# Kernel tuning notes

Measured on AMD Instinct MI355X. Metric: run time of the kernel, lower is better.

## Reference

```python
import jax, jax.numpy as jnp
import numpy as np

B, T, C = 8, 2048, 1024
NEG_BIG = -1e30  # exp(NEG_BIG - row_max) underflows to exactly 0 in fp32


def setup_inputs() -> dict:
    key = jax.random.key(0)
    k1, k2 = jax.random.split(key)
    x = jax.random.normal(k1, (B, T, C), dtype=jnp.float32)
    # nn.Linear weight, shape [out, in]; forward computes x @ W^T
    W_H = jax.random.normal(k2, (C, C), dtype=jnp.float32) * (1.0 / np.sqrt(C))
    return {"x": x, "W_H": W_H}


def reference(x, W_H):
    Tdim = x.shape[1]
    xH = jnp.einsum('btc,dc->btd', x, W_H)          # H(x) = x @ W^T, [B,T,C]
    scores = jnp.einsum('btc,bsc->bts', x, xH)       # bilinear scores, [B,T,T]
    # tril_plus_one=True -> strictly-lower-triangular mask (diagonal=-1)
    mask = jnp.tril(jnp.ones((Tdim, Tdim), dtype=bool), k=-1)
    scores = jnp.where(mask, scores, NEG_BIG)
    wei = jax.nn.softmax(scores, axis=-1)            # fully-masked rows -> uniform, zeroed below
    all_masked = ~mask.any(axis=-1)                  # [T], True for row 0
    wei = jnp.where(all_masked[None, :, None], 0.0, wei)
    out = jnp.einsum('bts,bsc->btc', wei, xH)
    return -out
```

## Files before the change

### kernel.cpp

```cpp
#include <hip/hip_runtime.h>
#include <stdint.h>

#define Bn 8
#define Tn 2048
#define Cn 1024
#define Mn (Bn * Tn)
#define NTRI 136

typedef __attribute__((ext_vector_type(4))) float f32x4;
typedef _Float16 f16;
typedef __attribute__((ext_vector_type(8))) _Float16 f16x8;
typedef uint16_t u16;
typedef uint32_t u32;

static __device__ __forceinline__ u16 f2h(float f) {
  union { f16 h; u16 u; } c; c.h = (f16)f; return c.u;
}
static __device__ __forceinline__ f32x4 mfmaH(f16x8 a, f16x8 b, f32x4 c) {
  return __builtin_amdgcn_mfma_f32_16x16x32_f16(a, b, c, 0, 0, 0);
}
static __device__ __forceinline__ void gld16(const void* g, void* l) {
  __builtin_amdgcn_global_load_lds(
      (const __attribute__((address_space(1))) u32*)g,
      (__attribute__((address_space(3))) u32*)l, 16, 0, 0);
}

__global__ __launch_bounds__(256) void ksplitW(const float* __restrict__ s,
                                               u16* __restrict__ hi) {
  size_t i = ((size_t)blockIdx.x * 256 + threadIdx.x) * 8;
  float4 a = *(const float4*)(s + i), b = *(const float4*)(s + i + 4);
  float f[8] = {a.x, a.y, a.z, a.w, b.x, b.y, b.z, b.w};
  union { u16 u[8]; uint4 v; } H;
#pragma unroll
  for (int j = 0; j < 8; ++j) H.u[j] = f2h(f[j]);
  *(uint4*)(hi + i) = H.v;
}

__global__ __launch_bounds__(256) void ksplitX(const float* __restrict__ s,
                                               u16* __restrict__ hi,
                                               u16* __restrict__ lo) {
  size_t i = ((size_t)blockIdx.x * 256 + threadIdx.x) * 8;
  float4 a = *(const float4*)(s + i), b = *(const float4*)(s + i + 4);
  float f[8] = {a.x, a.y, a.z, a.w, b.x, b.y, b.z, b.w};
  union { u16 u[8]; uint4 v; } H, L;
#pragma unroll
  for (int j = 0; j < 8; ++j) {
    f16 h = (f16)f[j];
    union { f16 h; u16 u; } ch; ch.h = h;
    H.u[j] = ch.u;
    L.u[j] = f2h(f[j] - (float)h);
  }
  *(uint4*)(hi + i) = H.v;
  *(uint4*)(lo + i) = L.v;
}

__global__ __launch_bounds__(256) void k1_xh(const u16* __restrict__ x_h,
                                             const u16* __restrict__ W_h,
                                             u16* __restrict__ xh) {
  __shared__ __align__(16) u16 Ah[8192], Bh[8192];
  const int tid = threadIdx.x;
  const int m0 = blockIdx.x * 128, n0 = blockIdx.y * 128;
  const int wave = tid >> 6, lane = tid & 63;
  const int wrow = (wave >> 1) * 64, wcol = (wave & 1) * 64;
  const int quad = lane >> 4, l16 = lane & 15;

  f32x4 acc[4][4] = {};

  for (int k0 = 0; k0 < Cn; k0 += 64) {
#pragma unroll
    for (int i = 0; i < 4; ++i) {
      int chunk = i * 256 + tid;
      int kk = chunk >> 9, row = (chunk >> 2) & 127, c8 = (chunk & 3) * 8;
      gld16(x_h + (size_t)(m0 + row) * Cn + k0 + kk * 32 + c8, Ah + chunk * 8);
      gld16(W_h + (size_t)(n0 + row) * Cn + k0 + kk * 32 + c8, Bh + chunk * 8);
    }
    __syncthreads();
#pragma unroll
    for (int kk = 0; kk < 2; ++kk) {
      f16x8 a[4], b[4];
#pragma unroll
      for (int i = 0; i < 4; ++i) {
        a[i] = *(const f16x8*)(Ah + kk * 4096 + (wrow + i * 16 + l16) * 32 + quad * 8);
        b[i] = *(const f16x8*)(Bh + kk * 4096 + (wcol + i * 16 + l16) * 32 + quad * 8);
      }
#pragma unroll
      for (int mi = 0; mi < 4; ++mi)
#pragma unroll
        for (int ni = 0; ni < 4; ++ni)
          acc[mi][ni] = mfmaH(a[mi], b[ni], acc[mi][ni]);
    }
    __syncthreads();
  }
#pragma unroll
  for (int mi = 0; mi < 4; ++mi)
#pragma unroll
    for (int ni = 0; ni < 4; ++ni)
#pragma unroll
      for (int r = 0; r < 4; ++r) {
        int row = wrow + mi * 16 + quad * 4 + r;
        int col = wcol + ni * 16 + l16;
        xh[(size_t)(m0 + row) * Cn + n0 + col] = f2h(acc[mi][ni][r]);
      }
}

__global__ __launch_bounds__(256) void k2_scores(const u16* __restrict__ x_h,
                                                 const u16* __restrict__ x_l,
                                                 const u16* __restrict__ xh,
                                                 u16* __restrict__ P,
                                                 float* __restrict__ mt,
                                                 float* __restrict__ lt) {
  __shared__ __align__(16) union {
    struct { u16 Ah[4096], Al[4096], Bh[4096]; } s;
    struct { float Mrow[2][128]; float Lrow[2][128]; } e;
  } u;
  const int tid = threadIdx.x;
  const int bL = blockIdx.y;
  const int lin = blockIdx.x;
  int qt = 0;
  while ((qt + 1) * (qt + 2) / 2 <= lin) qt++;
  const int st = lin - qt * (qt + 1) / 2;
  const int t0 = qt * 128, s0 = st * 128;
  const int wave = tid >> 6, lane = tid & 63;
  const int wrow = (wave >> 1) * 64, wcol = (wave & 1) * 64;
  const int quad = lane >> 4, l16 = lane & 15;
  const int srow = tid >> 2, skc = (tid & 3) * 8;

  f32x4 acc[4][4] = {};
  const size_t aoff = ((size_t)bL * Tn + t0 + srow) * Cn + skc;
  const size_t boff = ((size_t)bL * Tn + s0 + srow) * Cn + skc;

  for (int k0 = 0; k0 < Cn; k0 += 32) {
#pragma unroll
    for (int i = 0; i < 2; ++i) {
      size_t ro = (size_t)i * 64 * Cn;
      int lo_ = i * 2048 + tid * 8;
      gld16(x_h + aoff + ro + k0, u.s.Ah + lo_);
      gld16(x_l + aoff + ro + k0, u.s.Al + lo_);
      gld16(xh + boff + ro + k0, u.s.Bh + lo_);
    }
    __syncthreads();
    f16x8 a_h[4], a_l[4], b_h[4];
#pragma unroll
    for (int i = 0; i < 4; ++i) {
      a_h[i] = *(const f16x8*)(u.s.Ah + (wrow + i * 16 + l16) * 32 + quad * 8);
      a_l[i] = *(const f16x8*)(u.s.Al + (wrow + i * 16 + l16) * 32 + quad * 8);
      b_h[i] = *(const f16x8*)(u.s.Bh + (wcol + i * 16 + l16) * 32 + quad * 8);
    }
#pragma unroll
    for (int mi = 0; mi < 4; ++mi)
#pragma unroll
      for (int ni = 0; ni < 4; ++ni) {
        acc[mi][ni] = mfmaH(a_h[mi], b_h[ni], acc[mi][ni]);
        acc[mi][ni] = mfmaH(a_l[mi], b_h[ni], acc[mi][ni]);
      }
    __syncthreads();
  }

  float rm[4][4];
#pragma unroll
  for (int mi = 0; mi < 4; ++mi)
#pragma unroll
    for (int r = 0; r < 4; ++r) {
      int row = wrow + mi * 16 + quad * 4 + r;
      float m = -1e30f;
#pragma unroll
      for (int ni = 0; ni < 4; ++ni) {
        int col = wcol + ni * 16 + l16;
        if (s0 + col >= t0 + row) acc[mi][ni][r] = -1e30f;
        m = fmaxf(m, acc[mi][ni][r]);
      }
      m = fmaxf(m, __shfl_xor(m, 1));
      m = fmaxf(m, __shfl_xor(m, 2));
      m = fmaxf(m, __shfl_xor(m, 4));
      m = fmaxf(m, __shfl_xor(m, 8));
      rm[mi][r] = m;
    }
  if (l16 == 0) {
#pragma unroll
    for (int mi = 0; mi < 4; ++mi)
#pragma unroll
      for (int r = 0; r < 4; ++r)
        u.e.Mrow[wave & 1][wrow + mi * 16 + quad * 4 + r] = rm[mi][r];
  }
  __syncthreads();
  float rs[4][4];
#pragma unroll
  for (int mi = 0; mi < 4; ++mi)
#pragma unroll
    for (int r = 0; r < 4; ++r) {
      int row = wrow + mi * 16 + quad * 4 + r;
      float m2 = fmaxf(u.e.Mrow[0][row], u.e.Mrow[1][row]);
      float s = 0.f;
#pragma unroll
      for (int ni = 0; ni < 4; ++ni) {
        int col = wcol + ni * 16 + l16;
        float p = (s0 + col < t0 + row) ? __expf(acc[mi][ni][r] - m2) : 0.0f;
        acc[mi][ni][r] = p;
        s += p;
      }
      s += __shfl_xor(s, 1);
      s += __shfl_xor(s, 2);
      s += __shfl_xor(s, 4);
      s += __shfl_xor(s, 8);
      rs[mi][r] = s;
      rm[mi][r] = m2;
    }
  if (l16 == 0) {
#pragma unroll
    for (int mi = 0; mi < 4; ++mi)
#pragma unroll
      for (int r = 0; r < 4; ++r)
        u.e.Lrow[wave & 1][wrow + mi * 16 + quad * 4 + r] = rs[mi][r];
  }
  __syncthreads();
  if ((wave & 1) == 0 && l16 == 0) {
#pragma unroll
    for (int mi = 0; mi < 4; ++mi)
#pragma unroll
      for (int r = 0; r < 4; ++r) {
        int row = wrow + mi * 16 + quad * 4 + r;
        size_t rI = (size_t)bL * Tn + t0 + row;
        mt[rI * 16 + st] = rm[mi][r];
        lt[rI * 16 + st] = u.e.Lrow[0][row] + u.e.Lrow[1][row];
      }
  }
  const size_t pbase = (size_t)(bL * NTRI + lin) * 16384;
#pragma unroll
  for (int mi = 0; mi < 4; ++mi)
#pragma unroll
    for (int ni = 0; ni < 4; ++ni)
#pragma unroll
      for (int r = 0; r < 4; ++r) {
        int row = wrow + mi * 16 + quad * 4 + r;
        int col = wcol + ni * 16 + l16;
        P[pbase + row * 128 + col] = f2h(acc[mi][ni][r]);
      }
}

__global__ __launch_bounds__(256) void k3_stats(const float* __restrict__ mt,
                                                const float* __restrict__ lt,
                                                float* __restrict__ Mr,
                                                float* __restrict__ Li) {
  int r = blockIdx.x * 256 + threadIdx.x;
  int t = r & (Tn - 1);
  int nt = (t == 0) ? 0 : (((t - 1) >> 7) + 1);
  float M = -1e30f;
  for (int i = 0; i < nt; ++i) M = fmaxf(M, mt[(size_t)r * 16 + i]);
  float L = 0.f;
  for (int i = 0; i < nt; ++i) L += lt[(size_t)r * 16 + i] * __expf(mt[(size_t)r * 16 + i] - M);
  Mr[r] = M;
  Li[r] = (L > 0.f) ? 1.f / L : 0.f;
}

__global__ __launch_bounds__(256) void ktr(const u16* __restrict__ src,
                                           u16* __restrict__ dst) {
  __shared__ __align__(16) u16 S[128 * 136];
  const int t0 = blockIdx.x * 128, c0 = blockIdx.y * 128, b = blockIdx.z;
  const int tid = threadIdx.x;
#pragma unroll
  for (int i = 0; i < 8; ++i) {
    int chunk = tid + i * 256;
    int row = chunk >> 4, c8 = (chunk & 15) * 8;
    uint4 v = *(const uint4*)(src + ((size_t)b * Tn + t0 + row) * Cn + c0 + c8);
    *(uint4*)(S + row * 136 + c8) = v;
  }
  __syncthreads();
#pragma unroll
  for (int i = 0; i < 8; ++i) {
    int chunk = tid + i * 256;
    int crow = chunk >> 4, t8 = (chunk & 15) * 8;
    union { u16 s[8]; uint4 v; } o;
#pragma unroll
    for (int j = 0; j < 8; ++j) o.s[j] = S[(t8 + j) * 136 + crow];
    *(uint4*)(dst + ((size_t)b * Cn + c0 + crow) * Tn + t0 + t8) = o.v;
  }
}

__global__ __launch_bounds__(256) void k4_out(const u16* __restrict__ P,
                                              const u16* __restrict__ xhT,
                                              const float* __restrict__ mt,
                                              const float* __restrict__ Mr,
                                              const float* __restrict__ Li,
                                              float* __restrict__ out) {
  __shared__ __align__(16) u16 Ap[8192], Bp[8192];
  const int tid = threadIdx.x;
  const int tt = 15 - blockIdx.x;
  const int cn = blockIdx.y, bL = blockIdx.z;
  const int t0 = tt * 128, c0 = cn * 128;
  const int wave = tid >> 6, lane = tid & 63;
  const int wrow = (wave >> 1) * 64, wcol = (wave & 1) * 64;
  const int quad = lane >> 4, l16 = lane & 15;

  f32x4 acc[4][4] = {};
  size_t rI[4]; float MrL[4], LiL[4];
#pragma unroll
  for (int mi = 0; mi < 4; ++mi) {
    rI[mi] = (size_t)bL * Tn + t0 + wrow + mi * 16 + l16;
    MrL[mi] = Mr[rI[mi]];
    LiL[mi] = Li[rI[mi]];
  }
  const size_t bbase = ((size_t)bL * Cn + c0) * Tn;

  for (int st = 0; st <= tt; ++st) {
    f16 ah[4];
#pragma unroll
    for (int mi = 0; mi < 4; ++mi)
      ah[mi] = (f16)(__expf(mt[rI[mi] * 16 + st] - MrL[mi]) * LiL[mi]);
    const size_t pbase = (size_t)(bL * NTRI + tt * (tt + 1) / 2 + st) * 16384;
#pragma unroll 1
    for (int kl = 0; kl < 128; kl += 64) {
#pragma unroll
      for (int i = 0; i < 4; ++i) {
        int chunk = i * 256 + tid;
        int kk = chunk >> 9, row = (chunk >> 2) & 127, c8 = (chunk & 3) * 8;
        gld16(P + pbase + (size_t)row * 128 + kl + kk * 32 + c8, Ap + chunk * 8);
        gld16(xhT + bbase + (size_t)row * Tn + st * 128 + kl + kk * 32 + c8, Bp + chunk * 8);
      }
      __syncthreads();
#pragma unroll
      for (int kk = 0; kk < 2; ++kk) {
        f16x8 a[4], b[4];
#pragma unroll
        for (int i = 0; i < 4; ++i) {
          a[i] = *(const f16x8*)(Ap + kk * 4096 + (wrow + i * 16 + l16) * 32 + quad * 8);
          f16x8 sv;
#pragma unroll
          for (int j = 0; j < 8; ++j) sv[j] = ah[i];
          a[i] = a[i] * sv;
          b[i] = *(const f16x8*)(Bp + kk * 4096 + (wcol + i * 16 + l16) * 32 + quad * 8);
        }
#pragma unroll
        for (int mi = 0; mi < 4; ++mi)
#pragma unroll
          for (int ni = 0; ni < 4; ++ni)
            acc[mi][ni] = mfmaH(a[mi], b[ni], acc[mi][ni]);
      }
      __syncthreads();
    }
  }
#pragma unroll
  for (int mi = 0; mi < 4; ++mi)
#pragma unroll
    for (int ni = 0; ni < 4; ++ni)
#pragma unroll
      for (int r = 0; r < 4; ++r) {
        int row = wrow + mi * 16 + quad * 4 + r;
        int col = wcol + ni * 16 + l16;
        out[((size_t)bL * Tn + t0 + row) * Cn + c0 + col] = -acc[mi][ni][r];
      }
}

extern "C" void kernel_launch(void* const* d_in, const int* in_sizes, int n_in,
                              void* d_out, int out_size, void* d_ws, size_t ws_size,
                              hipStream_t stream) {
  (void)in_sizes; (void)n_in; (void)out_size;
  const float* x = (const float*)d_in[0];
  const float* W = (const float*)d_in[1];
  float* out = (float*)d_out;

  const size_t FULL_NEED = 3ull * Mn * Cn * 2 + (size_t)Bn * NTRI * 16384 * 2 +
                           (size_t)Cn * Cn * 2 + 2ull * Mn * 16 * 4 + 2ull * Mn * 4;
  const int nch = (ws_size >= FULL_NEED) ? 1 : 2;
  const int nb = Bn / nch;
  const size_t rowsC = (size_t)nb * Tn;
  const size_t sA = rowsC * Cn * 2;

  char* p = (char*)d_ws;
  u16* x_h = (u16*)p; p += sA;
  u16* xLT = (u16*)p; p += sA;
  u16* xh  = (u16*)p; p += sA;
  u16* Pp  = (u16*)p; p += (size_t)nb * NTRI * 16384 * 2;
  u16* W_h = (u16*)p; p += (size_t)Cn * Cn * 2;
  float* mt = (float*)p; p += rowsC * 16 * 4;
  float* lt = (float*)p; p += rowsC * 16 * 4;
  float* Mr = (float*)p; p += rowsC * 4;
  float* Li = (float*)p; p += rowsC * 4;

  dim3 blk(256);
  ksplitW<<<dim3(Cn * Cn / 2048), blk, 0, stream>>>(W, W_h);
  for (int c = 0; c < nch; ++c) {
    const float* xc = x + (size_t)c * rowsC * Cn;
    float* oc = out + (size_t)c * rowsC * Cn;
    ksplitX<<<dim3((u32)(rowsC * Cn / 2048)), blk, 0, stream>>>(xc, x_h, xLT);
    k1_xh<<<dim3((u32)(rowsC / 128), Cn / 128), blk, 0, stream>>>(x_h, W_h, xh);
    k2_scores<<<dim3(NTRI, nb), blk, 0, stream>>>(x_h, xLT, xh, Pp, mt, lt);
    k3_stats<<<dim3((u32)(rowsC / 256)), blk, 0, stream>>>(mt, lt, Mr, Li);
    ktr<<<dim3(Tn / 128, Cn / 128, nb), blk, 0, stream>>>(xh, xLT);
    k4_out<<<dim3(16, Cn / 128, nb), blk, 0, stream>>>(Pp, xLT, mt, Mr, Li, oc);
  }
}
```

Baseline: 427.1 us.

## Widen GEMM tiles to 128x256 and repack score tiles as 128x256 blocks

Widens the N dimension of the xH projection, score and output GEMMs from 128 to 256, so each wave computes a 64x128 tile and reuses each A fragment across twice as many MFMAs. The triangular score tiling becomes 128x256 blocks (72 per batch instead of 136), which changes the P buffer layout, the per-row stats stride and the softmax reduction. The output kernel loops over 256-wide key blocks with a clipped trip count. The workspace-size fallback to two batch chunks is removed, and the larger accumulators raise register and LDS use, which may lower occupancy and waste work on masked half-blocks.

```diff
diff --git a/kernel.cpp b/kernel.cpp
--- a/kernel.cpp
+++ b/kernel.cpp
@@ -5,7 +5,8 @@
 #define Tn 2048
 #define Cn 1024
 #define Mn (Bn * Tn)
-#define NTRI 136
+#define NTB 72
+#define NST 8
 
 typedef __attribute__((ext_vector_type(4))) float f32x4;
 typedef _Float16 f16;
@@ -23,6 +24,10 @@
   __builtin_amdgcn_global_load_lds(
       (const __attribute__((address_space(1))) u32*)g,
       (__attribute__((address_space(3))) u32*)l, 16, 0, 0);
+}
+static __device__ __forceinline__ int tri_off(int qt) {
+  int a = qt >> 1;
+  return (qt & 1) ? (a + 1) * (a + 1) : a * (a + 1);
 }
 
 __global__ __launch_bounds__(256) void ksplitW(const float* __restrict__ s,
@@ -57,36 +62,42 @@
 __global__ __launch_bounds__(256) void k1_xh(const u16* __restrict__ x_h,
                                              const u16* __restrict__ W_h,
                                              u16* __restrict__ xh) {
-  __shared__ __align__(16) u16 Ah[8192], Bh[8192];
+  __shared__ __align__(16) u16 Ah[8192], Bh[16384];
   const int tid = threadIdx.x;
-  const int m0 = blockIdx.x * 128, n0 = blockIdx.y * 128;
+  const int m0 = blockIdx.x * 128, n0 = blockIdx.y * 256;
   const int wave = tid >> 6, lane = tid & 63;
-  const int wrow = (wave >> 1) * 64, wcol = (wave & 1) * 64;
+  const int wrow = (wave >> 1) * 64, wcol = (wave & 1) * 128;
   const int quad = lane >> 4, l16 = lane & 15;
 
-  f32x4 acc[4][4] = {};
+  f32x4 acc[4][8] = {};
 
   for (int k0 = 0; k0 < Cn; k0 += 64) {
 #pragma unroll
     for (int i = 0; i < 4; ++i) {
       int chunk = i * 256 + tid;
       int kk = chunk >> 9, row = (chunk >> 2) & 127, c8 = (chunk & 3) * 8;
-      gld16(x_h + (size_t)(m0 + row) * Cn + k0 + kk * 32 + c8, Ah + chunk * 8);
-      gld16(W_h + (size_t)(n0 + row) * Cn + k0 + kk * 32 + c8, Bh + chunk * 8);
+      gld16(x_h + (size_t)(m0 + row) * Cn + k0 + kk * 32 + c8, Ah + kk * 4096 + row * 32 + c8);
+    }
+#pragma unroll
+    for (int i = 0; i < 8; ++i) {
+      int chunk = i * 256 + tid;
+      int kk = chunk >> 10, row = (chunk >> 2) & 255, c8 = (chunk & 3) * 8;
+      gld16(W_h + (size_t)(n0 + row) * Cn + k0 + kk * 32 + c8, Bh + kk * 8192 + row * 32 + c8);
     }
     __syncthreads();
 #pragma unroll
     for (int kk = 0; kk < 2; ++kk) {
-      f16x8 a[4], b[4];
-#pragma unroll
-      for (int i = 0; i < 4; ++i) {
+      f16x8 a[4], b[8];
+#pragma unroll
+      for (int i = 0; i < 4; ++i)
         a[i] = *(const f16x8*)(Ah + kk * 4096 + (wrow + i * 16 + l16) * 32 + quad * 8);
-        b[i] = *(const f16x8*)(Bh + kk * 4096 + (wcol + i * 16 + l16) * 32 + quad * 8);
-      }
+#pragma unroll
+      for (int j = 0; j < 8; ++j)
+        b[j] = *(const f16x8*)(Bh + kk * 8192 + (wcol + j * 16 + l16) * 32 + quad * 8);
 #pragma unroll
       for (int mi = 0; mi < 4; ++mi)
 #pragma unroll
-        for (int ni = 0; ni < 4; ++ni)
+        for (int ni = 0; ni < 8; ++ni)
           acc[mi][ni] = mfmaH(a[mi], b[ni], acc[mi][ni]);
     }
     __syncthreads();
@@ -94,7 +105,7 @@
 #pragma unroll
   for (int mi = 0; mi < 4; ++mi)
 #pragma unroll
-    for (int ni = 0; ni < 4; ++ni)
+    for (int ni = 0; ni < 8; ++ni)
 #pragma unroll
       for (int r = 0; r < 4; ++r) {
         int row = wrow + mi * 16 + quad * 4 + r;
@@ -110,48 +121,53 @@
                                                  float* __restrict__ mt,
                                                  float* __restrict__ lt) {
   __shared__ __align__(16) union {
-    struct { u16 Ah[4096], Al[4096], Bh[4096]; } s;
+    struct { u16 Ah[4096], Al[4096], Bh[8192]; } s;
     struct { float Mrow[2][128]; float Lrow[2][128]; } e;
   } u;
   const int tid = threadIdx.x;
   const int bL = blockIdx.y;
   const int lin = blockIdx.x;
-  int qt = 0;
-  while ((qt + 1) * (qt + 2) / 2 <= lin) qt++;
-  const int st = lin - qt * (qt + 1) / 2;
-  const int t0 = qt * 128, s0 = st * 128;
+  int qt = 0, base = 0;
+  while (base + (qt >> 1) + 1 <= lin) { base += (qt >> 1) + 1; qt++; }
+  const int st2 = lin - base;
+  const int t0 = qt * 128, s0 = st2 * 256;
   const int wave = tid >> 6, lane = tid & 63;
-  const int wrow = (wave >> 1) * 64, wcol = (wave & 1) * 64;
+  const int wrow = (wave >> 1) * 64, wcol = (wave & 1) * 128;
   const int quad = lane >> 4, l16 = lane & 15;
-  const int srow = tid >> 2, skc = (tid & 3) * 8;
-
-  f32x4 acc[4][4] = {};
-  const size_t aoff = ((size_t)bL * Tn + t0 + srow) * Cn + skc;
-  const size_t boff = ((size_t)bL * Tn + s0 + srow) * Cn + skc;
+
+  f32x4 acc[4][8] = {};
 
   for (int k0 = 0; k0 < Cn; k0 += 32) {
 #pragma unroll
     for (int i = 0; i < 2; ++i) {
-      size_t ro = (size_t)i * 64 * Cn;
-      int lo_ = i * 2048 + tid * 8;
-      gld16(x_h + aoff + ro + k0, u.s.Ah + lo_);
-      gld16(x_l + aoff + ro + k0, u.s.Al + lo_);
-      gld16(xh + boff + ro + k0, u.s.Bh + lo_);
+      int chunk = i * 256 + tid;
+      int row = chunk >> 2, c8 = (chunk & 3) * 8;
+      size_t g = ((size_t)bL * Tn + t0 + row) * Cn + k0 + c8;
+      gld16(x_h + g, u.s.Ah + row * 32 + c8);
+      gld16(x_l + g, u.s.Al + row * 32 + c8);
+    }
+#pragma unroll
+    for (int i = 0; i < 4; ++i) {
+      int chunk = i * 256 + tid;
+      int row = chunk >> 2, c8 = (chunk & 3) * 8;
+      gld16(xh + ((size_t)bL * Tn + s0 + row) * Cn + k0 + c8, u.s.Bh + row * 32 + c8);
     }
     __syncthreads();
-    f16x8 a_h[4], a_l[4], b_h[4];
+    f16x8 a_h[4], a_l[4], b[8];
 #pragma unroll
     for (int i = 0; i < 4; ++i) {
       a_h[i] = *(const f16x8*)(u.s.Ah + (wrow + i * 16 + l16) * 32 + quad * 8);
       a_l[i] = *(const f16x8*)(u.s.Al + (wrow + i * 16 + l16) * 32 + quad * 8);
-      b_h[i] = *(const f16x8*)(u.s.Bh + (wcol + i * 16 + l16) * 32 + quad * 8);
-    }
+    }
+#pragma unroll
+    for (int j = 0; j < 8; ++j)
+      b[j] = *(const f16x8*)(u.s.Bh + (wcol + j * 16 + l16) * 32 + quad * 8);
 #pragma unroll
     for (int mi = 0; mi < 4; ++mi)
 #pragma unroll
-      for (int ni = 0; ni < 4; ++ni) {
-        acc[mi][ni] = mfmaH(a_h[mi], b_h[ni], acc[mi][ni]);
-        acc[mi][ni] = mfmaH(a_l[mi], b_h[ni], acc[mi][ni]);
+      for (int ni = 0; ni < 8; ++ni) {
+        acc[mi][ni] = mfmaH(a_h[mi], b[ni], acc[mi][ni]);
+        acc[mi][ni] = mfmaH(a_l[mi], b[ni], acc[mi][ni]);
       }
     __syncthreads();
   }
@@ -164,7 +180,7 @@
       int row = wrow + mi * 16 + quad * 4 + r;
       float m = -1e30f;
 #pragma unroll
-      for (int ni = 0; ni < 4; ++ni) {
+      for (int ni = 0; ni < 8; ++ni) {
         int col = wcol + ni * 16 + l16;
         if (s0 + col >= t0 + row) acc[mi][ni][r] = -1e30f;
         m = fmaxf(m, acc[mi][ni][r]);
@@ -192,7 +208,7 @@
       float m2 = fmaxf(u.e.Mrow[0][row], u.e.Mrow[1][row]);
       float s = 0.f;
 #pragma unroll
-      for (int ni = 0; ni < 4; ++ni) {
+      for (int ni = 0; ni < 8; ++ni) {
         int col = wcol + ni * 16 + l16;
         float p = (s0 + col < t0 + row) ? __expf(acc[mi][ni][r] - m2) : 0.0f;
         acc[mi][ni][r] = p;
@@ -220,20 +236,20 @@
       for (int r = 0; r < 4; ++r) {
         int row = wrow + mi * 16 + quad * 4 + r;
         size_t rI = (size_t)bL * Tn + t0 + row;
-        mt[rI * 16 + st] = rm[mi][r];
-        lt[rI * 16 + st] = u.e.Lrow[0][row] + u.e.Lrow[1][row];
-      }
-  }
-  const size_t pbase = (size_t)(bL * NTRI + lin) * 16384;
+        mt[rI * NST + st2] = rm[mi][r];
+        lt[rI * NST + st2] = u.e.Lrow[0][row] + u.e.Lrow[1][row];
+      }
+  }
+  const size_t pbase = (size_t)(bL * NTB + lin) * 32768;
 #pragma unroll
   for (int mi = 0; mi < 4; ++mi)
 #pragma unroll
-    for (int ni = 0; ni < 4; ++ni)
+    for (int ni = 0; ni < 8; ++ni)
 #pragma unroll
       for (int r = 0; r < 4; ++r) {
         int row = wrow + mi * 16 + quad * 4 + r;
         int col = wcol + ni * 16 + l16;
-        P[pbase + row * 128 + col] = f2h(acc[mi][ni][r]);
+        P[pbase + row * 256 + col] = f2h(acc[mi][ni][r]);
       }
 }
 
@@ -243,11 +259,11 @@
                                                 float* __restrict__ Li) {
   int r = blockIdx.x * 256 + threadIdx.x;
   int t = r & (Tn - 1);
-  int nt = (t == 0) ? 0 : (((t - 1) >> 7) + 1);
+  int nt = (t == 0) ? 0 : (((t - 1) >> 8) + 1);
   float M = -1e30f;
-  for (int i = 0; i < nt; ++i) M = fmaxf(M, mt[(size_t)r * 16 + i]);
+  for (int i = 0; i < nt; ++i) M = fmaxf(M, mt[(size_t)r * NST + i]);
   float L = 0.f;
-  for (int i = 0; i < nt; ++i) L += lt[(size_t)r * 16 + i] * __expf(mt[(size_t)r * 16 + i] - M);
+  for (int i = 0; i < nt; ++i) L += lt[(size_t)r * NST + i] * __expf(mt[(size_t)r * NST + i] - M);
   Mr[r] = M;
   Li[r] = (L > 0.f) ? 1.f / L : 0.f;
 }
@@ -282,16 +298,16 @@
                                               const float* __restrict__ Mr,
                                               const float* __restrict__ Li,
                                               float* __restrict__ out) {
-  __shared__ __align__(16) u16 Ap[8192], Bp[8192];
+  __shared__ __align__(16) u16 Ap[8192], Bp[16384];
   const int tid = threadIdx.x;
   const int tt = 15 - blockIdx.x;
   const int cn = blockIdx.y, bL = blockIdx.z;
-  const int t0 = tt * 128, c0 = cn * 128;
+  const int t0 = tt * 128, c0 = cn * 256;
   const int wave = tid >> 6, lane = tid & 63;
-  const int wrow = (wave >> 1) * 64, wcol = (wave & 1) * 64;
+  const int wrow = (wave >> 1) * 64, wcol = (wave & 1) * 128;
   const int quad = lane >> 4, l16 = lane & 15;
 
-  f32x4 acc[4][4] = {};
+  f32x4 acc[4][8] = {};
   size_t rI[4]; float MrL[4], LiL[4];
 #pragma unroll
   for (int mi = 0; mi < 4; ++mi) {
@@ -300,26 +316,35 @@
     LiL[mi] = Li[rI[mi]];
   }
   const size_t bbase = ((size_t)bL * Cn + c0) * Tn;
-
-  for (int st = 0; st <= tt; ++st) {
+  const int off = tri_off(tt);
+  const int kend = (tt + 1) * 128;
+
+  for (int st2 = 0; st2 <= (tt >> 1); ++st2) {
     f16 ah[4];
 #pragma unroll
     for (int mi = 0; mi < 4; ++mi)
-      ah[mi] = (f16)(__expf(mt[rI[mi] * 16 + st] - MrL[mi]) * LiL[mi]);
-    const size_t pbase = (size_t)(bL * NTRI + tt * (tt + 1) / 2 + st) * 16384;
+      ah[mi] = (f16)(__expf(mt[rI[mi] * NST + st2] - MrL[mi]) * LiL[mi]);
+    const size_t pbase = (size_t)(bL * NTB + off + st2) * 32768;
+    const int klim = min(256, kend - st2 * 256);
 #pragma unroll 1
-    for (int kl = 0; kl < 128; kl += 64) {
+    for (int kl = 0; kl < klim; kl += 64) {
 #pragma unroll
       for (int i = 0; i < 4; ++i) {
         int chunk = i * 256 + tid;
         int kk = chunk >> 9, row = (chunk >> 2) & 127, c8 = (chunk & 3) * 8;
-        gld16(P + pbase + (size_t)row * 128 + kl + kk * 32 + c8, Ap + chunk * 8);
-        gld16(xhT + bbase + (size_t)row * Tn + st * 128 + kl + kk * 32 + c8, Bp + chunk * 8);
+        gld16(P + pbase + (size_t)row * 256 + kl + kk * 32 + c8, Ap + kk * 4096 + row * 32 + c8);
+      }
+#pragma unroll
+      for (int i = 0; i < 8; ++i) {
+        int chunk = i * 256 + tid;
+        int kk = chunk >> 10, row = (chunk >> 2) & 255, c8 = (chunk & 3) * 8;
+        gld16(xhT + bbase + (size_t)row * Tn + st2 * 256 + kl + kk * 32 + c8,
+              Bp + kk * 8192 + row * 32 + c8);
       }
       __syncthreads();
 #pragma unroll
       for (int kk = 0; kk < 2; ++kk) {
-        f16x8 a[4], b[4];
+        f16x8 a[4], b[8];
 #pragma unroll
         for (int i = 0; i < 4; ++i) {
           a[i] = *(const f16x8*)(Ap + kk * 4096 + (wrow + i * 16 + l16) * 32 + quad * 8);
@@ -327,12 +352,14 @@
 #pragma unroll
           for (int j = 0; j < 8; ++j) sv[j] = ah[i];
           a[i] = a[i] * sv;
-          b[i] = *(const f16x8*)(Bp + kk * 4096 + (wcol + i * 16 + l16) * 32 + quad * 8);
         }
 #pragma unroll
+        for (int j = 0; j < 8; ++j)
+          b[j] = *(const f16x8*)(Bp + kk * 8192 + (wcol + j * 16 + l16) * 32 + quad * 8);
+#pragma unroll
         for (int mi = 0; mi < 4; ++mi)
 #pragma unroll
-          for (int ni = 0; ni < 4; ++ni)
+          for (int ni = 0; ni < 8; ++ni)
             acc[mi][ni] = mfmaH(a[mi], b[ni], acc[mi][ni]);
       }
       __syncthreads();
@@ -341,7 +368,7 @@
 #pragma unroll
   for (int mi = 0; mi < 4; ++mi)
 #pragma unroll
-    for (int ni = 0; ni < 4; ++ni)
+    for (int ni = 0; ni < 8; ++ni)
 #pragma unroll
       for (int r = 0; r < 4; ++r) {
         int row = wrow + mi * 16 + quad * 4 + r;
@@ -353,39 +380,28 @@
 extern "C" void kernel_launch(void* const* d_in, const int* in_sizes, int n_in,
                               void* d_out, int out_size, void* d_ws, size_t ws_size,
                               hipStream_t stream) {
-  (void)in_sizes; (void)n_in; (void)out_size;
+  (void)in_sizes; (void)n_in; (void)out_size; (void)ws_size;
   const float* x = (const float*)d_in[0];
   const float* W = (const float*)d_in[1];
   float* out = (float*)d_out;
 
-  const size_t FULL_NEED = 3ull * Mn * Cn * 2 + (size_t)Bn * NTRI * 16384 * 2 +
-                           (size_t)Cn * Cn * 2 + 2ull * Mn * 16 * 4 + 2ull * Mn * 4;
-  const int nch = (ws_size >= FULL_NEED) ? 1 : 2;
-  const int nb = Bn / nch;
-  const size_t rowsC = (size_t)nb * Tn;
-  const size_t sA = rowsC * Cn * 2;
-
   char* p = (char*)d_ws;
-  u16* x_h = (u16*)p; p += sA;
-  u16* xLT = (u16*)p; p += sA;
-  u16* xh  = (u16*)p; p += sA;
-  u16* Pp  = (u16*)p; p += (size_t)nb * NTRI * 16384 * 2;
+  u16* x_h = (u16*)p; p += (size_t)Mn * Cn * 2;
+  u16* xLT = (u16*)p; p += (size_t)Mn * Cn * 2;
+  u16* xh  = (u16*)p; p += (size_t)Mn * Cn * 2;
+  u16* Pp  = (u16*)p; p += (size_t)Bn * NTB * 32768 * 2;
   u16* W_h = (u16*)p; p += (size_t)Cn * Cn * 2;
-  float* mt = (float*)p; p += rowsC * 16 * 4;
-  float* lt = (float*)p; p += rowsC * 16 * 4;
-  float* Mr = (float*)p; p += rowsC * 4;
-  float* Li = (float*)p; p += rowsC * 4;
+  float* mt = (float*)p; p += (size_t)Mn * NST * 4;
+  float* lt = (float*)p; p += (size_t)Mn * NST * 4;
+  float* Mr = (float*)p; p += (size_t)Mn * 4;
+  float* Li = (float*)p; p += (size_t)Mn * 4;
 
   dim3 blk(256);
-  ksplitW<<<dim3(Cn * Cn / 2048), blk, 0, stream>>>(W, W_h);
-  for (int c = 0; c < nch; ++c) {
-    const float* xc = x + (size_t)c * rowsC * Cn;
-    float* oc = out + (size_t)c * rowsC * Cn;
-    ksplitX<<<dim3((u32)(rowsC * Cn / 2048)), blk, 0, stream>>>(xc, x_h, xLT);
-    k1_xh<<<dim3((u32)(rowsC / 128), Cn / 128), blk, 0, stream>>>(x_h, W_h, xh);
-    k2_scores<<<dim3(NTRI, nb), blk, 0, stream>>>(x_h, xLT, xh, Pp, mt, lt);
-    k3_stats<<<dim3((u32)(rowsC / 256)), blk, 0, stream>>>(mt, lt, Mr, Li);
-    ktr<<<dim3(Tn / 128, Cn / 128, nb), blk, 0, stream>>>(xh, xLT);
-    k4_out<<<dim3(16, Cn / 128, nb), blk, 0, stream>>>(Pp, xLT, mt, Mr, Li, oc);
-  }
-}
+  ksplitW<<<dim3((Cn * Cn) / 2048), blk, 0, stream>>>(W, W_h);
+  ksplitX<<<dim3((u32)(((size_t)Mn * Cn) / 2048)), blk, 0, stream>>>(x, x_h, xLT);
+  k1_xh<<<dim3(Mn / 128, Cn / 256), blk, 0, stream>>>(x_h, W_h, xh);
+  k2_scores<<<dim3(NTB, Bn), blk, 0, stream>>>(x_h, xLT, xh, Pp, mt, lt);
+  k3_stats<<<dim3(Mn / 256), blk, 0, stream>>>(mt, lt, Mr, Li);
+  ktr<<<dim3(Tn / 128, Cn / 128, Bn), blk, 0, stream>>>(xh, xLT);
+  k4_out<<<dim3(16, Cn / 256, Bn), blk, 0, stream>>>(Pp, xLT, mt, Mr, Li, out);
+}
```

Measured after the change: 495.0 us. +15.9%, slower.
